# Performance work log

Measured on AMD Instinct MI355X. Metric: run time of the kernel, lower is better.

The kernel has to match this reference:

```python
import jax, jax.numpy as jnp
import numpy as np

N_KNN = 20
BN_EPS = 1e-5
LRELU_SLOPE = 0.2


def setup_inputs() -> dict:
    key = jax.random.key(0)
    k1, k2, k3 = jax.random.split(key, 3)
    B, C, N = 4, 3, 8192
    x = jax.random.normal(k1, (B, C, N), dtype=jnp.float32)
    # Conv2d(1, 16, 1): weight [16,1,1,1] -> flatten to [16]; bias [16]
    conv_w = jax.random.normal(k2, (16,), dtype=jnp.float32) * (1.0 / np.sqrt(1.0))
    conv_b = jax.random.normal(k3, (16,), dtype=jnp.float32) * 0.01
    gamma = jnp.ones((16,), dtype=jnp.float32)
    beta = jnp.zeros((16,), dtype=jnp.float32)
    return {"x": x, "conv_w": conv_w, "conv_b": conv_b, "gamma": gamma, "beta": beta}


def reference(x, conv_w, conv_b, gamma, beta):
    # x: [B, C, N]
    pts = jnp.transpose(x, (0, 2, 1))  # [B, N, C]
    sq = jnp.sum(pts * pts, axis=-1)  # [B, N]
    # pairwise squared distances, clamped for numerical safety
    d2 = sq[:, :, None] + sq[:, None, :] - 2.0 * jnp.einsum("bnc,bmc->bnm", pts, pts)
    d2 = jnp.maximum(d2, 0.0)
    # safe sqrt: zero gradient at zero distance (matches torch.cdist behavior)
    dist = jnp.where(d2 > 0, jnp.sqrt(jnp.where(d2 > 0, d2, 1.0)), 0.0)  # [B, N, N]
    # k smallest distances = k largest of negated
    neg_topk, _ = jax.lax.top_k(-dist, N_KNN)
    knn = -neg_topk  # [B, N, K], ascending
    # 1x1 conv (1 -> 16 channels): feat[b,c,n,k] = w[c]*knn[b,n,k] + b[c]
    feat = knn[:, None, :, :] * conv_w[None, :, None, None] + conv_b[None, :, None, None]  # [B,16,N,K]
    # BatchNorm2d in training mode: per-channel stats over (B, N, K), biased variance
    mean = jnp.mean(feat, axis=(0, 2, 3), keepdims=True)
    var = jnp.mean((feat - mean) ** 2, axis=(0, 2, 3), keepdims=True)
    xhat = (feat - mean) * jax.lax.rsqrt(var + BN_EPS)
    y = gamma[None, :, None, None] * xhat + beta[None, :, None, None]
    # LeakyReLU(0.2)
    y = jnp.where(y >= 0, y, LRELU_SLOPE * y)
    # max over k neighbors
    return jnp.max(y, axis=-1)  # [B, 16, N]
```

## Files before the change

kernel.cpp:

```cpp
#include <hip/hip_runtime.h>
#include <stdint.h>

#define NPTS  8192
#define NB    4
#define KNN   20
#define NROWS (NB * NPTS)
#define MTOTF 655360.0f
#define WPB   8
#define BLK   (WPB * 64)
#define SLICE (NPTS / WPB)
#define HALF  (NPTS / 2)
#define SLICE2 (HALF / WPB)
#define LSTR  (KNN + 1)
#define CAP   12
#define CAP2  16
#define NEG_INF -3.0e38f

__device__ __forceinline__ float med3f(float a, float b, float c) {
    return __builtin_amdgcn_fmed3f(a, b, c);
}

__device__ __forceinline__ unsigned enc_f(float f) {
    unsigned u = __float_as_uint(f);
    return (u & 0x80000000u) ? ~u : (u | 0x80000000u);
}
__device__ __forceinline__ float dec_f(unsigned u) {
    return __uint_as_float((u & 0x80000000u) ? (u & 0x7fffffffu) : ~u);
}

__device__ __forceinline__ void insert_t(float arr[KNN], float t) {
#pragma unroll
    for (int j = KNN - 1; j > 0; --j) arr[j] = med3f(t, arr[j - 1], arr[j]);
    arr[0] = fmaxf(arr[0], t);
}

__device__ __forceinline__ void flush_buf(float arr[KNN], int& cnt,
    const float* bufw, int lane, unsigned* threshS) {
#pragma unroll
    for (int s = 0; s < CAP; ++s) {
        const float v = bufw[s * 64 + lane];
        insert_t(arr, (s < cnt) ? v : NEG_INF);
    }
    cnt = 0;
    atomicMax(&threshS[lane], enc_f(arr[KNN - 1]));
}

__device__ __forceinline__ void flush_dyn(float arr[KNN], int& cnt,
    const float* bufw, int lane, unsigned* threshS) {
#pragma unroll
    for (int s0 = 0; s0 < CAP2; s0 += 4) {
        if (__any(cnt > s0)) {
#pragma unroll
            for (int s = s0; s < s0 + 4; ++s) {
                const float v = bufw[s * 64 + lane];
                insert_t(arr, (s < cnt) ? v : NEG_INF);
            }
        }
    }
    cnt = 0;
    atomicMax(&threshS[lane], enc_f(arr[KNN - 1]));
}

__device__ __forceinline__ void finalize_row(
    float arr[KNN], float px, float py, float pz, int row, int lane,
    float* __restrict__ kmaxA, float* __restrict__ kminA, float* __restrict__ acc)
{
    const float pn2 = px * px + py * py + pz * pz;
    float sum = 0.f, sum2 = 0.f, dmin = 0.f, dmax = 0.f;
#pragma unroll
    for (int k = 0; k < KNN; ++k) {
        float d2 = fmaxf(fmaf(-2.f, arr[k], pn2), 0.f);
        float d = sqrtf(d2);
        sum += d; sum2 += d2;
        if (k == 0) dmin = d;
        dmax = d;
    }
    kmaxA[row] = dmax;
    kminA[row] = dmin;
#pragma unroll
    for (int o = 32; o; o >>= 1) {
        sum  += __shfl_down(sum,  o, 64);
        sum2 += __shfl_down(sum2, o, 64);
    }
    if (lane == 0) { atomicAdd(acc, sum); atomicAdd(acc + 1, sum2); }
}

__global__ __launch_bounds__(256) void prep_kernel(
    const float* __restrict__ x, float4* __restrict__ tile4, float* __restrict__ acc)
{
    const int i = blockIdx.x * 256 + threadIdx.x;
    const int b = i >> 13;
    const int m = i & (NPTS - 1);
    const float* xb = x + b * 3 * NPTS;
    const float qx = xb[m], qy = xb[NPTS + m], qz = xb[2 * NPTS + m];
    tile4[i] = make_float4(qx, qy, qz, -0.5f * (qx * qx + qy * qy + qz * qz));
    if (i < 2) acc[i] = 0.f;
}

__global__ __launch_bounds__(BLK, 8) void knn_split_kernel(
    const float* __restrict__ x, const float4* __restrict__ tile4,
    float* __restrict__ part)
{
    __shared__ float shmem[(WPB - 1) * 64 * LSTR];
    __shared__ unsigned threshS[64];

    const int tid  = threadIdx.x;
    const int lane = tid & 63;
    const int wave = __builtin_amdgcn_readfirstlane(tid >> 6);
    const int rb   = blockIdx.x >> 1;
    const int half = blockIdx.x & 1;
    const int rowBase = rb * 64;
    const int row  = rowBase + lane;
    const int b    = rowBase >> 13;
    const int n    = row & (NPTS - 1);
    const float* xb = x + b * 3 * NPTS;

    const float px = xb[n];
    const float py = xb[NPTS + n];
    const float pz = xb[2 * NPTS + n];

    if (tid < 64) threshS[tid] = enc_f(NEG_INF);

    float arr[KNN];
#pragma unroll
    for (int j = 0; j < KNN; ++j) arr[j] = NEG_INF;

    float* bufw = shmem + wave * (CAP2 * 64);
    __syncthreads();

    const float4* __restrict__ tp = tile4 + b * NPTS + half * HALF + wave * SLICE2;

#pragma unroll 8
    for (int i = 0; i < 32; ++i) {
        const float4 q = tp[i];
        insert_t(arr, fmaf(q.x, px, fmaf(q.y, py, fmaf(q.z, pz, q.w))));
    }
    atomicMax(&threshS[lane], enc_f(arr[KNN - 1]));

    int cnt = 0;
    for (int c = 1; c < SLICE2 / 32; ++c) {
        float th = dec_f(*(volatile unsigned*)(threshS + lane));
        const float4* tq = tp + c * 32;
        for (int g = 0; g < 8; ++g) {
#pragma unroll
            for (int u = 0; u < 4; ++u) {
                const float4 q = tq[g * 4 + u];
                const float t = fmaf(q.x, px, fmaf(q.y, py, fmaf(q.z, pz, q.w)));
                bufw[cnt * 64 + lane] = t;
                cnt += (t > th);
            }
            if (__any(cnt > CAP2 - 4)) {
                flush_dyn(arr, cnt, bufw, lane, threshS);
                th = dec_f(*(volatile unsigned*)(threshS + lane));
            }
        }
    }
    if (__any(cnt > 0)) flush_dyn(arr, cnt, bufw, lane, threshS);
    __syncthreads();

    if (wave > 0) {
        float* dst = shmem + ((wave - 1) * 64 + lane) * LSTR;
#pragma unroll
        for (int j = 0; j < KNN; ++j) dst[j] = arr[j];
    }
    __syncthreads();

    if (wave == 0) {
        for (int wsrc = 0; wsrc < WPB - 1; ++wsrc) {
            const float* src = shmem + (wsrc * 64 + lane) * LSTR;
#pragma unroll
            for (int k = 0; k < KNN; ++k) insert_t(arr, src[k]);
        }
        float4* dst = (float4*)(part + (row * 2 + half) * KNN);
#pragma unroll
        for (int k = 0; k < KNN; k += 4)
            dst[k >> 2] = make_float4(arr[k], arr[k + 1], arr[k + 2], arr[k + 3]);
    }
}

__global__ __launch_bounds__(256) void merge_kernel(
    const float* __restrict__ x, const float* __restrict__ part,
    float* __restrict__ kmaxA, float* __restrict__ kminA, float* __restrict__ acc)
{
    const int r = blockIdx.x * 256 + threadIdx.x;
    const int lane = threadIdx.x & 63;
    const int b = r >> 13;
    const int n = r & (NPTS - 1);
    const float* xb = x + b * 3 * NPTS;
    const float px = xb[n];
    const float py = xb[NPTS + n];
    const float pz = xb[2 * NPTS + n];

    const float4* pA = (const float4*)(part + r * 2 * KNN);
    float arr[KNN];
#pragma unroll
    for (int k = 0; k < KNN; k += 4) {
        const float4 v = pA[k >> 2];
        arr[k] = v.x; arr[k + 1] = v.y; arr[k + 2] = v.z; arr[k + 3] = v.w;
    }
#pragma unroll
    for (int k = 0; k < KNN; k += 4) {
        const float4 v = pA[(KNN + k) >> 2];
        insert_t(arr, v.x); insert_t(arr, v.y); insert_t(arr, v.z); insert_t(arr, v.w);
    }
    finalize_row(arr, px, py, pz, r, lane, kmaxA, kminA, acc);
}

__global__ __launch_bounds__(BLK, 8) void knn_kernel(
    const float* __restrict__ x, const float4* __restrict__ tile4,
    float* __restrict__ kmaxA, float* __restrict__ kminA, float* __restrict__ acc)
{
    __shared__ float shmem[(WPB - 1) * 64 * LSTR];
    __shared__ unsigned threshS[64];

    const int tid  = threadIdx.x;
    const int lane = tid & 63;
    const int wave = __builtin_amdgcn_readfirstlane(tid >> 6);
    const int rowBase = blockIdx.x * 64;
    const int row  = rowBase + lane;
    const int b    = rowBase >> 13;
    const int n    = row & (NPTS - 1);
    const float* xb = x + b * 3 * NPTS;

    const float px = xb[n];
    const float py = xb[NPTS + n];
    const float pz = xb[2 * NPTS + n];

    if (tid < 64) threshS[tid] = enc_f(NEG_INF);

    float arr[KNN];
#pragma unroll
    for (int j = 0; j < KNN; ++j) arr[j] = NEG_INF;

    float* bufw = shmem + wave * (CAP * 64);
    int cnt = 0;
    __syncthreads();

    const float4* __restrict__ tp = tile4 + b * NPTS + wave * SLICE;
    float th = NEG_INF;
    for (int c = 0; c < SLICE / 32; ++c) {
        th = dec_f(*(volatile unsigned*)(threshS + lane));
        const float4* tq = tp + c * 32;
        for (int g = 0; g < 8; ++g) {
#pragma unroll
            for (int u = 0; u < 4; ++u) {
                const float4 q = tq[g * 4 + u];
                const float t = fmaf(q.x, px, fmaf(q.y, py, fmaf(q.z, pz, q.w)));
                if (t > th) { bufw[cnt * 64 + lane] = t; ++cnt; }
            }
            if (__any(cnt > CAP - 4)) {
                flush_buf(arr, cnt, bufw, lane, threshS);
                th = dec_f(*(volatile unsigned*)(threshS + lane));
            }
        }
    }
    if (__any(cnt > 0)) flush_buf(arr, cnt, bufw, lane, threshS);
    __syncthreads();

    if (wave > 0) {
        float* dst = shmem + ((wave - 1) * 64 + lane) * LSTR;
#pragma unroll
        for (int j = 0; j < KNN; ++j) dst[j] = arr[j];
    }
    __syncthreads();

    if (wave == 0) {
        for (int wsrc = 0; wsrc < WPB - 1; ++wsrc) {
            const float* src = shmem + (wsrc * 64 + lane) * LSTR;
#pragma unroll
            for (int k = 0; k < KNN; ++k) insert_t(arr, src[k]);
        }
        finalize_row(arr, px, py, pz, row, lane, kmaxA, kminA, acc);
    }
}

__global__ __launch_bounds__(BLK) void knn_kernel_lds(
    const float* __restrict__ x,
    float* __restrict__ kmaxA, float* __restrict__ kminA, float* __restrict__ acc)
{
    __shared__ float4 tile[2048];
    __shared__ float  lists[(WPB - 1) * 64 * LSTR];

    const int tid  = threadIdx.x;
    const int lane = tid & 63;
    const int wave = tid >> 6;
    const int rowBase = blockIdx.x * 64;
    const int row  = rowBase + lane;
    const int b    = rowBase >> 13;
    const int n    = row & (NPTS - 1);
    const float* xb = x + b * 3 * NPTS;

    const float px = xb[n];
    const float py = xb[NPTS + n];
    const float pz = xb[2 * NPTS + n];

    float arr[KNN];
#pragma unroll
    for (int j = 0; j < KNN; ++j) arr[j] = NEG_INF;

    for (int t0 = 0; t0 < NPTS; t0 += 2048) {
        __syncthreads();
        const int i4 = tid * 4;
        const float4 qx4 = *(const float4*)(xb + t0 + i4);
        const float4 qy4 = *(const float4*)(xb + NPTS + t0 + i4);
        const float4 qz4 = *(const float4*)(xb + 2 * NPTS + t0 + i4);
        tile[i4 + 0] = make_float4(qx4.x, qy4.x, qz4.x, -0.5f * (qx4.x*qx4.x + qy4.x*qy4.x + qz4.x*qz4.x));
        tile[i4 + 1] = make_float4(qx4.y, qy4.y, qz4.y, -0.5f * (qx4.y*qx4.y + qy4.y*qy4.y + qz4.y*qz4.y));
        tile[i4 + 2] = make_float4(qx4.z, qy4.z, qz4.z, -0.5f * (qx4.z*qx4.z + qy4.z*qy4.z + qz4.z*qz4.z));
        tile[i4 + 3] = make_float4(qx4.w, qy4.w, qz4.w, -0.5f * (qx4.w*qx4.w + qy4.w*qy4.w + qz4.w*qz4.w));
        __syncthreads();
        const float4* base = tile + wave * 256;
#pragma unroll 4
        for (int i = 0; i < 256; ++i) {
            const float4 q = base[i];
            float t = fmaf(q.x, px, fmaf(q.y, py, fmaf(q.z, pz, q.w)));
            insert_t(arr, t);
        }
    }
    __syncthreads();

    if (wave > 0) {
        float* dst = lists + ((wave - 1) * 64 + lane) * LSTR;
#pragma unroll
        for (int j = 0; j < KNN; ++j) dst[j] = arr[j];
    }
    __syncthreads();

    if (wave == 0) {
        for (int wsrc = 0; wsrc < WPB - 1; ++wsrc) {
            const float* src = lists + (wsrc * 64 + lane) * LSTR;
#pragma unroll
            for (int k = 0; k < KNN; ++k) insert_t(arr, src[k]);
        }
        finalize_row(arr, px, py, pz, row, lane, kmaxA, kminA, acc);
    }
}

__global__ __launch_bounds__(256) void out_kernel(
    const float* __restrict__ kmaxA, const float* __restrict__ kminA,
    const float* __restrict__ acc,
    const float* __restrict__ w, const float* __restrict__ gamma,
    const float* __restrict__ beta, float* __restrict__ out)
{
    const int r = blockIdx.x * 256 + threadIdx.x;
    const int b = r >> 13;
    const int n = r & (NPTS - 1);
    const float mu  = acc[0] * (1.0f / MTOTF);
    float var = acc[1] * (1.0f / MTOTF) - mu * mu;
    var = fmaxf(var, 0.f);
    const float kmax = kmaxA[r];
    const float kmin = kminA[r];
#pragma unroll
    for (int c = 0; c < 16; ++c) {
        const float wc = w[c];
        const float a = gamma[c] * wc * rsqrtf(wc * wc * var + 1e-5f);
        const float d = beta[c] - a * mu;
        float v = a * (a >= 0.f ? kmax : kmin) + d;
        v = (v >= 0.f) ? v : 0.2f * v;
        out[(b * 16 + c) * NPTS + n] = v;
    }
}

extern "C" void kernel_launch(void* const* d_in, const int* in_sizes, int n_in,
                              void* d_out, int out_size, void* d_ws, size_t ws_size,
                              hipStream_t stream)
{
    const float* x     = (const float*)d_in[0];
    const float* w     = (const float*)d_in[1];
    const float* gamma = (const float*)d_in[3];
    const float* beta  = (const float*)d_in[4];
    float* out = (float*)d_out;
    float* ws  = (float*)d_ws;

    float* kmaxA = ws;
    float* kminA = ws + NROWS;
    float* acc   = ws + 2 * NROWS;
    float4* tile4 = (float4*)(ws + 2 * NROWS + 4);
    float* part = ws + (2 * NROWS + 4) + 4 * NROWS;
    const size_t need_tile  = (size_t)(2 * NROWS + 4) * 4 + (size_t)NROWS * 16;
    const size_t need_split = need_tile + (size_t)NROWS * 2 * KNN * 4;

    if (ws_size >= need_split) {
        prep_kernel<<<NROWS / 256, 256, 0, stream>>>(x, tile4, acc);
        knn_split_kernel<<<2 * (NROWS / 64), BLK, 0, stream>>>(x, tile4, part);
        merge_kernel<<<NROWS / 256, 256, 0, stream>>>(x, part, kmaxA, kminA, acc);
    } else if (ws_size >= need_tile) {
        prep_kernel<<<NROWS / 256, 256, 0, stream>>>(x, tile4, acc);
        knn_kernel<<<NROWS / 64, BLK, 0, stream>>>(x, tile4, kmaxA, kminA, acc);
    } else {
        prep_kernel<<<1, 256, 0, stream>>>(x, tile4, acc);
        knn_kernel_lds<<<NROWS / 64, BLK, 0, stream>>>(x, kmaxA, kminA, acc);
    }
    out_kernel<<<NROWS / 256, 256, 0, stream>>>(kmaxA, kminA, acc, w, gamma, beta, out);
}
```

Measured before the change: 202.5 us.

## Replace per-wave flush buffers with shared hot list drained round-robin

Each row's top-k now lives in one shared ladder in LDS with a shared threshold. Candidates above the threshold go into a fixed per-wave hot buffer, and one wave per phase drains all waves' buffers into the ladder while the others keep scanning. Overflow falls back to per-lane register lists that are merged at the end. The aim is to cut the repeated per-wave insertion sorts and the final 8-way merge, at the cost of 16 block barriers, a serial drain by one wave each phase, and benign races on the hot buffer.

Result: slower. 428.5 us (+111.6%).

```diff
diff --git a/kernel.cpp b/kernel.cpp
--- a/kernel.cpp
+++ b/kernel.cpp
@@ -13,8 +13,11 @@
 #define SLICE2 (HALF / WPB)
 #define LSTR  (KNN + 1)
 #define CAP   12
-#define CAP2  16
+#define CW    14
+#define WARM  32
+#define NPH   15
 #define NEG_INF -3.0e38f
+#define SENTU 0x7fbfffffu
 
 __device__ __forceinline__ float med3f(float a, float b, float c) {
     return __builtin_amdgcn_fmed3f(a, b, c);
@@ -45,20 +48,40 @@
     atomicMax(&threshS[lane], enc_f(arr[KNN - 1]));
 }
 
-__device__ __forceinline__ void flush_dyn(float arr[KNN], int& cnt,
-    const float* bufw, int lane, unsigned* threshS) {
-#pragma unroll
-    for (int s0 = 0; s0 < CAP2; s0 += 4) {
-        if (__any(cnt > s0)) {
-#pragma unroll
-            for (int s = s0; s < s0 + 4; ++s) {
-                const float v = bufw[s * 64 + lane];
-                insert_t(arr, (s < cnt) ? v : NEG_INF);
-            }
-        }
-    }
-    cnt = 0;
-    atomicMax(&threshS[lane], enc_f(arr[KNN - 1]));
+__device__ __forceinline__ void drain_rows(
+    const float* hotS, float* ladS, float* threshS, int* curS, int lane)
+{
+    float lad[KNN];
+#pragma unroll
+    for (int k = 0; k < KNN; ++k) lad[k] = ladS[lane * LSTR + k];
+    for (int w = 0; w < WPB; ++w) {
+        int cur = curS[w * 64 + lane];
+        while (true) {
+            bool act = cur < CW;
+            float v = NEG_INF;
+            if (act) v = hotS[(w * CW + cur) * 64 + lane];
+            act = act && (__float_as_uint(v) != SENTU);
+            if (!__any(act)) break;
+            if (act) { insert_t(lad, v); ++cur; }
+        }
+        curS[w * 64 + lane] = cur;
+    }
+#pragma unroll
+    for (int k = 0; k < KNN; ++k) ladS[lane * LSTR + k] = lad[k];
+    threshS[lane] = lad[KNN - 1];
+}
+
+__device__ __forceinline__ void merge_arr_to_lad(
+    float* ladS, float* threshS, const float arr[KNN], int lane)
+{
+    float lad[KNN];
+#pragma unroll
+    for (int k = 0; k < KNN; ++k) lad[k] = ladS[lane * LSTR + k];
+#pragma unroll
+    for (int k = 0; k < KNN; ++k) insert_t(lad, arr[k]);
+#pragma unroll
+    for (int k = 0; k < KNN; ++k) ladS[lane * LSTR + k] = lad[k];
+    threshS[lane] = lad[KNN - 1];
 }
 
 __device__ __forceinline__ void finalize_row(
@@ -97,12 +120,15 @@
     if (i < 2) acc[i] = 0.f;
 }
 
-__global__ __launch_bounds__(BLK, 8) void knn_split_kernel(
+__global__ __launch_bounds__(BLK, 8) void knn_hot_kernel(
     const float* __restrict__ x, const float4* __restrict__ tile4,
     float* __restrict__ part)
 {
-    __shared__ float shmem[(WPB - 1) * 64 * LSTR];
-    __shared__ unsigned threshS[64];
+    __shared__ float    hotS[WPB * CW * 64];
+    __shared__ float    ladS[64 * LSTR];
+    __shared__ float    threshS[64];
+    __shared__ int      curS[WPB * 64];
+    __shared__ unsigned dirtyS;
 
     const int tid  = threadIdx.x;
     const int lane = tid & 63;
@@ -114,67 +140,83 @@
     const int b    = rowBase >> 13;
     const int n    = row & (NPTS - 1);
     const float* xb = x + b * 3 * NPTS;
-
     const float px = xb[n];
     const float py = xb[NPTS + n];
     const float pz = xb[2 * NPTS + n];
 
-    if (tid < 64) threshS[tid] = enc_f(NEG_INF);
+    for (int i = tid; i < WPB * CW * 64; i += BLK) ((unsigned*)hotS)[i] = SENTU;
+    for (int i = tid; i < WPB * 64; i += BLK) curS[i] = 0;
+    if (tid == 0) dirtyS = 0u;
 
     float arr[KNN];
 #pragma unroll
     for (int j = 0; j < KNN; ++j) arr[j] = NEG_INF;
 
-    float* bufw = shmem + wave * (CAP2 * 64);
-    __syncthreads();
-
     const float4* __restrict__ tp = tile4 + b * NPTS + half * HALF + wave * SLICE2;
 
-#pragma unroll 8
-    for (int i = 0; i < 32; ++i) {
+#pragma unroll 4
+    for (int i = 0; i < WARM; ++i) {
         const float4 q = tp[i];
         insert_t(arr, fmaf(q.x, px, fmaf(q.y, py, fmaf(q.z, pz, q.w))));
     }
-    atomicMax(&threshS[lane], enc_f(arr[KNN - 1]));
-
+
+    for (int w = 0; w < WPB; ++w) {
+        __syncthreads();
+        if (wave == w) {
+            if (w == 0) {
+#pragma unroll
+                for (int k = 0; k < KNN; ++k) ladS[lane * LSTR + k] = arr[k];
+                threshS[lane] = arr[KNN - 1];
+            } else {
+                merge_arr_to_lad(ladS, threshS, arr, lane);
+            }
+        }
+    }
+    __syncthreads();
+
+#pragma unroll
+    for (int j = 0; j < KNN; ++j) arr[j] = NEG_INF;
+
+    float* secp = &hotS[(wave * CW) * 64 + lane];
     int cnt = 0;
-    for (int c = 1; c < SLICE2 / 32; ++c) {
-        float th = dec_f(*(volatile unsigned*)(threshS + lane));
-        const float4* tq = tp + c * 32;
-        for (int g = 0; g < 8; ++g) {
-#pragma unroll
-            for (int u = 0; u < 4; ++u) {
-                const float4 q = tq[g * 4 + u];
-                const float t = fmaf(q.x, px, fmaf(q.y, py, fmaf(q.z, pz, q.w)));
-                bufw[cnt * 64 + lane] = t;
-                cnt += (t > th);
+
+    for (int p = 0; p < NPH; ++p) {
+        const float th = threshS[lane];
+        if (wave == (p & 7))
+            drain_rows(hotS, ladS, threshS, curS, lane);
+        const float4* tq = tp + WARM + p * 32;
+#pragma unroll 4
+        for (int i = 0; i < 32; ++i) {
+            const float4 q = tq[i];
+            const float t = fmaf(q.x, px, fmaf(q.y, py, fmaf(q.z, pz, q.w)));
+            if (t > th) {
+                if (cnt < CW) { secp[cnt * 64] = t; ++cnt; }
+                else { insert_t(arr, t); atomicOr(&dirtyS, 1u); }
             }
-            if (__any(cnt > CAP2 - 4)) {
-                flush_dyn(arr, cnt, bufw, lane, threshS);
-                th = dec_f(*(volatile unsigned*)(threshS + lane));
-            }
-        }
-    }
-    if (__any(cnt > 0)) flush_dyn(arr, cnt, bufw, lane, threshS);
-    __syncthreads();
-
-    if (wave > 0) {
-        float* dst = shmem + ((wave - 1) * 64 + lane) * LSTR;
-#pragma unroll
-        for (int j = 0; j < KNN; ++j) dst[j] = arr[j];
+        }
+        __syncthreads();
+    }
+
+    if (wave == 7) drain_rows(hotS, ladS, threshS, curS, lane);
+    __syncthreads();
+
+    if (dirtyS) {
+        for (int w = 0; w < WPB; ++w) {
+            __syncthreads();
+            if (wave == w && __any(arr[0] != NEG_INF))
+                merge_arr_to_lad(ladS, threshS, arr, lane);
+        }
     }
     __syncthreads();
 
     if (wave == 0) {
-        for (int wsrc = 0; wsrc < WPB - 1; ++wsrc) {
-            const float* src = shmem + (wsrc * 64 + lane) * LSTR;
-#pragma unroll
-            for (int k = 0; k < KNN; ++k) insert_t(arr, src[k]);
-        }
+        float o[KNN];
+#pragma unroll
+        for (int k = 0; k < KNN; ++k) o[k] = ladS[lane * LSTR + k];
         float4* dst = (float4*)(part + (row * 2 + half) * KNN);
 #pragma unroll
         for (int k = 0; k < KNN; k += 4)
-            dst[k >> 2] = make_float4(arr[k], arr[k + 1], arr[k + 2], arr[k + 3]);
+            dst[k >> 2] = make_float4(o[k], o[k + 1], o[k + 2], o[k + 3]);
     }
 }
 
@@ -382,7 +424,7 @@
 
     if (ws_size >= need_split) {
         prep_kernel<<<NROWS / 256, 256, 0, stream>>>(x, tile4, acc);
-        knn_split_kernel<<<2 * (NROWS / 64), BLK, 0, stream>>>(x, tile4, part);
+        knn_hot_kernel<<<2 * (NROWS / 64), BLK, 0, stream>>>(x, tile4, part);
         merge_kernel<<<NROWS / 256, 256, 0, stream>>>(x, part, kmaxA, kminA, acc);
     } else if (ws_size >= need_tile) {
         prep_kernel<<<NROWS / 256, 256, 0, stream>>>(x, tile4, acc);
```

## Pack candidate points in pairs for packed FMA and tree-merge wave results

Applied to the files above, without the earlier changes.

Prep now writes candidate points as interleaved pairs (x0,x1,y0,y1 / z0,z1,w0,w1) so the KNN kernel can score two candidates with packed two-wide FMAs. Pairs are staged and filtered together against the threshold using the max of the two scores, and flushed with a smaller per-wave buffer. The final cross-wave merge becomes a log-depth tree instead of wave 0 serially merging seven lists. This aims to cut the distance arithmetic and the serial merge tail. The cost is more extra inserts when only one element of a pair passes, plus more block barriers.

New measurement: 212.6 us. +5.0%, slower.

```diff
diff --git a/kernel.cpp b/kernel.cpp
--- a/kernel.cpp
+++ b/kernel.cpp
@@ -13,11 +13,24 @@
 #define SLICE2 (HALF / WPB)
 #define LSTR  (KNN + 1)
 #define CAP   12
-#define CAP2  16
+#define CW2   8
+#define PWARM 16
+#define PPH   16
+#define NPH2  ((SLICE2 / 2 - PWARM) / PPH)
 #define NEG_INF -3.0e38f
+
+typedef float f32x2 __attribute__((ext_vector_type(2)));
 
 __device__ __forceinline__ float med3f(float a, float b, float c) {
     return __builtin_amdgcn_fmed3f(a, b, c);
+}
+
+__device__ __forceinline__ f32x2 fma2(f32x2 a, f32x2 b, f32x2 c) {
+#if __has_builtin(__builtin_elementwise_fma)
+    return __builtin_elementwise_fma(a, b, c);
+#else
+    f32x2 r; r.x = fmaf(a.x, b.x, c.x); r.y = fmaf(a.y, b.y, c.y); return r;
+#endif
 }
 
 __device__ __forceinline__ unsigned enc_f(float f) {
@@ -45,15 +58,17 @@
     atomicMax(&threshS[lane], enc_f(arr[KNN - 1]));
 }
 
-__device__ __forceinline__ void flush_dyn(float arr[KNN], int& cnt,
-    const float* bufw, int lane, unsigned* threshS) {
-#pragma unroll
-    for (int s0 = 0; s0 < CAP2; s0 += 4) {
+__device__ __forceinline__ void flush_pairs(float arr[KNN], int& cnt,
+    const f32x2* secp, int lane, unsigned* threshS) {
+#pragma unroll
+    for (int s0 = 0; s0 < CW2; s0 += 2) {
         if (__any(cnt > s0)) {
 #pragma unroll
-            for (int s = s0; s < s0 + 4; ++s) {
-                const float v = bufw[s * 64 + lane];
-                insert_t(arr, (s < cnt) ? v : NEG_INF);
+            for (int s = s0; s < s0 + 2; ++s) {
+                const f32x2 v = secp[s * 64];
+                const bool a = (s < cnt);
+                insert_t(arr, a ? v.x : NEG_INF);
+                insert_t(arr, a ? v.y : NEG_INF);
             }
         }
     }
@@ -97,12 +112,31 @@
     if (i < 2) acc[i] = 0.f;
 }
 
-__global__ __launch_bounds__(BLK, 8) void knn_split_kernel(
+__global__ __launch_bounds__(256) void prep_pair_kernel(
+    const float* __restrict__ x, float4* __restrict__ tile4, float* __restrict__ acc)
+{
+    const int p = blockIdx.x * 256 + threadIdx.x;
+    const int b = p >> 12;
+    const int j = p & (NPTS / 2 - 1);
+    const float* xb = x + b * 3 * NPTS;
+    const f32x2 xx = *(const f32x2*)(xb + 2 * j);
+    const f32x2 yy = *(const f32x2*)(xb + NPTS + 2 * j);
+    const f32x2 zz = *(const f32x2*)(xb + 2 * NPTS + 2 * j);
+    const float w0 = -0.5f * (xx.x * xx.x + yy.x * yy.x + zz.x * zz.x);
+    const float w1 = -0.5f * (xx.y * xx.y + yy.y * yy.y + zz.y * zz.y);
+    tile4[2 * p + 0] = make_float4(xx.x, xx.y, yy.x, yy.y);
+    tile4[2 * p + 1] = make_float4(zz.x, zz.y, w0, w1);
+    if (p < 2) acc[p] = 0.f;
+}
+
+__global__ __launch_bounds__(BLK, 8) void knn_pk_kernel(
     const float* __restrict__ x, const float4* __restrict__ tile4,
     float* __restrict__ part)
 {
-    __shared__ float shmem[(WPB - 1) * 64 * LSTR];
+    __shared__ __align__(16) char smem[WPB * CW2 * 64 * sizeof(f32x2)];
     __shared__ unsigned threshS[64];
+    f32x2* hot = (f32x2*)smem;
+    float* ml  = (float*)smem;
 
     const int tid  = threadIdx.x;
     const int lane = tid & 63;
@@ -114,63 +148,91 @@
     const int b    = rowBase >> 13;
     const int n    = row & (NPTS - 1);
     const float* xb = x + b * 3 * NPTS;
-
     const float px = xb[n];
     const float py = xb[NPTS + n];
     const float pz = xb[2 * NPTS + n];
+    const f32x2 px2 = {px, px}, py2 = {py, py}, pz2 = {pz, pz};
 
     if (tid < 64) threshS[tid] = enc_f(NEG_INF);
 
     float arr[KNN];
 #pragma unroll
     for (int j = 0; j < KNN; ++j) arr[j] = NEG_INF;
-
-    float* bufw = shmem + wave * (CAP2 * 64);
-    __syncthreads();
-
-    const float4* __restrict__ tp = tile4 + b * NPTS + half * HALF + wave * SLICE2;
-
-#pragma unroll 8
-    for (int i = 0; i < 32; ++i) {
-        const float4 q = tp[i];
-        insert_t(arr, fmaf(q.x, px, fmaf(q.y, py, fmaf(q.z, pz, q.w))));
+    __syncthreads();
+
+    const f32x2* __restrict__ q2 = (const f32x2*)tile4;
+    const int pbase = b * (NPTS / 2) + half * (HALF / 2) + wave * (SLICE2 / 2);
+
+#pragma unroll 4
+    for (int i = 0; i < PWARM; ++i) {
+        const f32x2* tq = q2 + 4 * (pbase + i);
+        const f32x2 r = fma2(tq[0], px2, fma2(tq[1], py2, fma2(tq[2], pz2, tq[3])));
+        insert_t(arr, r.x);
+        insert_t(arr, r.y);
     }
     atomicMax(&threshS[lane], enc_f(arr[KNN - 1]));
 
+    f32x2* secp = hot + (wave * CW2) * 64 + lane;
     int cnt = 0;
-    for (int c = 1; c < SLICE2 / 32; ++c) {
+
+    for (int p = 0; p < NPH2; ++p) {
         float th = dec_f(*(volatile unsigned*)(threshS + lane));
-        const float4* tq = tp + c * 32;
-        for (int g = 0; g < 8; ++g) {
+        const f32x2* tq = q2 + 4 * (pbase + PWARM + p * PPH);
+        for (int g = 0; g < 4; ++g) {
 #pragma unroll
             for (int u = 0; u < 4; ++u) {
-                const float4 q = tq[g * 4 + u];
-                const float t = fmaf(q.x, px, fmaf(q.y, py, fmaf(q.z, pz, q.w)));
-                bufw[cnt * 64 + lane] = t;
-                cnt += (t > th);
+                const int j = g * 4 + u;
+                const f32x2 ax = tq[4 * j + 0];
+                const f32x2 ay = tq[4 * j + 1];
+                const f32x2 az = tq[4 * j + 2];
+                const f32x2 aw = tq[4 * j + 3];
+                const f32x2 r = fma2(ax, px2, fma2(ay, py2, fma2(az, pz2, aw)));
+                secp[cnt * 64] = r;
+                cnt += (fmaxf(r.x, r.y) > th);
             }
-            if (__any(cnt > CAP2 - 4)) {
-                flush_dyn(arr, cnt, bufw, lane, threshS);
+            if (__any(cnt > CW2 - 4)) {
+                flush_pairs(arr, cnt, secp, lane, threshS);
                 th = dec_f(*(volatile unsigned*)(threshS + lane));
             }
         }
     }
-    if (__any(cnt > 0)) flush_dyn(arr, cnt, bufw, lane, threshS);
-    __syncthreads();
-
-    if (wave > 0) {
-        float* dst = shmem + ((wave - 1) * 64 + lane) * LSTR;
-#pragma unroll
-        for (int j = 0; j < KNN; ++j) dst[j] = arr[j];
-    }
-    __syncthreads();
-
+    if (__any(cnt > 0)) flush_pairs(arr, cnt, secp, lane, threshS);
+    __syncthreads();
+
+    if (wave & 1) {
+        float* d = ml + (wave >> 1) * (64 * LSTR) + lane * LSTR;
+#pragma unroll
+        for (int k = 0; k < KNN; ++k) d[k] = arr[k];
+    }
+    __syncthreads();
+    if (!(wave & 1)) {
+        const float* s = ml + (wave >> 1) * (64 * LSTR) + lane * LSTR;
+#pragma unroll
+        for (int k = 0; k < KNN; ++k) insert_t(arr, s[k]);
+    }
+    __syncthreads();
+    if (!(wave & 1) && (wave & 2)) {
+        float* d = ml + (wave >> 2) * (64 * LSTR) + lane * LSTR;
+#pragma unroll
+        for (int k = 0; k < KNN; ++k) d[k] = arr[k];
+    }
+    __syncthreads();
+    if ((wave & 3) == 0) {
+        const float* s = ml + (wave >> 2) * (64 * LSTR) + lane * LSTR;
+#pragma unroll
+        for (int k = 0; k < KNN; ++k) insert_t(arr, s[k]);
+    }
+    __syncthreads();
+    if (wave == 4) {
+        float* d = ml + lane * LSTR;
+#pragma unroll
+        for (int k = 0; k < KNN; ++k) d[k] = arr[k];
+    }
+    __syncthreads();
     if (wave == 0) {
-        for (int wsrc = 0; wsrc < WPB - 1; ++wsrc) {
-            const float* src = shmem + (wsrc * 64 + lane) * LSTR;
-#pragma unroll
-            for (int k = 0; k < KNN; ++k) insert_t(arr, src[k]);
-        }
+        const float* s = ml + lane * LSTR;
+#pragma unroll
+        for (int k = 0; k < KNN; ++k) insert_t(arr, s[k]);
         float4* dst = (float4*)(part + (row * 2 + half) * KNN);
 #pragma unroll
         for (int k = 0; k < KNN; k += 4)
@@ -381,8 +443,8 @@
     const size_t need_split = need_tile + (size_t)NROWS * 2 * KNN * 4;
 
     if (ws_size >= need_split) {
-        prep_kernel<<<NROWS / 256, 256, 0, stream>>>(x, tile4, acc);
-        knn_split_kernel<<<2 * (NROWS / 64), BLK, 0, stream>>>(x, tile4, part);
+        prep_pair_kernel<<<NROWS / 512, 256, 0, stream>>>(x, tile4, acc);
+        knn_pk_kernel<<<2 * (NROWS / 64), BLK, 0, stream>>>(x, tile4, part);
         merge_kernel<<<NROWS / 256, 256, 0, stream>>>(x, part, kmaxA, kminA, acc);
     } else if (ws_size >= need_tile) {
         prep_kernel<<<NROWS / 256, 256, 0, stream>>>(x, tile4, acc);
```

## Fuse prep, split KNN, merge and output into one cooperative kernel

Applied to the files above, without the earlier changes.

Adds a cooperative mega-kernel that runs the prep, split KNN search, merge/finalize and output phases in one launch, separated by grid-wide syncs. It tries the cooperative launch first and falls back to the old multi-kernel path if that launch fails. The goal is to remove the launch overhead and gaps between the four kernels. The cost is that NGRID=1024 blocks of 512 threads must all be resident at once, which limits occupancy and adds grid-sync overhead. If residency is not possible the launch fails and the old path runs.

New measurement: 507.1 us. 150% more time.

```diff
diff --git a/kernel.cpp b/kernel.cpp
--- a/kernel.cpp
+++ b/kernel.cpp
@@ -1,5 +1,8 @@
 #include <hip/hip_runtime.h>
+#include <hip/hip_cooperative_groups.h>
 #include <stdint.h>
+
+namespace cg = cooperative_groups;
 
 #define NPTS  8192
 #define NB    4
@@ -14,6 +17,7 @@
 #define LSTR  (KNN + 1)
 #define CAP   12
 #define CAP2  16
+#define NGRID (2 * (NROWS / 64))
 #define NEG_INF -3.0e38f
 
 __device__ __forceinline__ float med3f(float a, float b, float c) {
@@ -84,6 +88,171 @@
     }
     if (lane == 0) { atomicAdd(acc, sum); atomicAdd(acc + 1, sum2); }
 }
+
+__global__ __launch_bounds__(BLK, 8) void mega_kernel(
+    const float* __restrict__ x, const float* __restrict__ w,
+    const float* __restrict__ gamma, const float* __restrict__ beta,
+    float4* __restrict__ tile4, float* __restrict__ part,
+    float* __restrict__ kmaxA, float* __restrict__ kminA,
+    float* __restrict__ acc, float* __restrict__ out)
+{
+    cg::grid_group grid = cg::this_grid();
+    __shared__ float shmem[WPB * CAP2 * 64];
+    __shared__ unsigned threshS[64];
+
+    const int tid  = threadIdx.x;
+    const int lane = tid & 63;
+    const int wave = __builtin_amdgcn_readfirstlane(tid >> 6);
+    const int blk  = blockIdx.x;
+
+    if (blk < NROWS / BLK) {
+        const int i = blk * BLK + tid;
+        const int b = i >> 13;
+        const int m = i & (NPTS - 1);
+        const float* xb = x + b * 3 * NPTS;
+        const float qx = xb[m], qy = xb[NPTS + m], qz = xb[2 * NPTS + m];
+        tile4[i] = make_float4(qx, qy, qz, -0.5f * (qx * qx + qy * qy + qz * qz));
+        if (i < 2) acc[i] = 0.f;
+    }
+    grid.sync();
+
+    {
+        const int rb   = blk >> 1;
+        const int half = blk & 1;
+        const int rowBase = rb * 64;
+        const int row  = rowBase + lane;
+        const int b    = rowBase >> 13;
+        const int n    = row & (NPTS - 1);
+        const float* xb = x + b * 3 * NPTS;
+        const float px = xb[n];
+        const float py = xb[NPTS + n];
+        const float pz = xb[2 * NPTS + n];
+
+        if (tid < 64) threshS[tid] = enc_f(NEG_INF);
+
+        float arr[KNN];
+#pragma unroll
+        for (int j = 0; j < KNN; ++j) arr[j] = NEG_INF;
+        float* bufw = shmem + wave * (CAP2 * 64);
+        __syncthreads();
+
+        const float4* __restrict__ tp = tile4 + b * NPTS + half * HALF + wave * SLICE2;
+
+#pragma unroll 8
+        for (int i = 0; i < 32; ++i) {
+            const float4 q = tp[i];
+            insert_t(arr, fmaf(q.x, px, fmaf(q.y, py, fmaf(q.z, pz, q.w))));
+        }
+        atomicMax(&threshS[lane], enc_f(arr[KNN - 1]));
+
+        int cnt = 0;
+        for (int c = 1; c < SLICE2 / 32; ++c) {
+            float th = dec_f(*(volatile unsigned*)(threshS + lane));
+            const float4* tq = tp + c * 32;
+            for (int g = 0; g < 8; ++g) {
+#pragma unroll
+                for (int u = 0; u < 4; ++u) {
+                    const float4 q = tq[g * 4 + u];
+                    const float t = fmaf(q.x, px, fmaf(q.y, py, fmaf(q.z, pz, q.w)));
+                    bufw[cnt * 64 + lane] = t;
+                    cnt += (t > th);
+                }
+                if (__any(cnt > CAP2 - 4)) {
+                    flush_dyn(arr, cnt, bufw, lane, threshS);
+                    th = dec_f(*(volatile unsigned*)(threshS + lane));
+                }
+            }
+        }
+        if (__any(cnt > 0)) flush_dyn(arr, cnt, bufw, lane, threshS);
+        __syncthreads();
+
+        float* ml = shmem;
+        if (wave & 1) {
+            float* d = ml + (wave >> 1) * (64 * LSTR) + lane * LSTR;
+#pragma unroll
+            for (int k = 0; k < KNN; ++k) d[k] = arr[k];
+        }
+        __syncthreads();
+        if (!(wave & 1)) {
+            const float* s = ml + (wave >> 1) * (64 * LSTR) + lane * LSTR;
+#pragma unroll
+            for (int k = 0; k < KNN; ++k) insert_t(arr, s[k]);
+        }
+        __syncthreads();
+        if (!(wave & 1) && (wave & 2)) {
+            float* d = ml + (wave >> 2) * (64 * LSTR) + lane * LSTR;
+#pragma unroll
+            for (int k = 0; k < KNN; ++k) d[k] = arr[k];
+        }
+        __syncthreads();
+        if ((wave & 3) == 0) {
+            const float* s = ml + (wave >> 2) * (64 * LSTR) + lane * LSTR;
+#pragma unroll
+            for (int k = 0; k < KNN; ++k) insert_t(arr, s[k]);
+        }
+        __syncthreads();
+        if (wave == 4) {
+            float* d = ml + lane * LSTR;
+#pragma unroll
+            for (int k = 0; k < KNN; ++k) d[k] = arr[k];
+        }
+        __syncthreads();
+        if (wave == 0) {
+            const float* s = ml + lane * LSTR;
+#pragma unroll
+            for (int k = 0; k < KNN; ++k) insert_t(arr, s[k]);
+            float4* dst = (float4*)(part + (row * 2 + half) * KNN);
+#pragma unroll
+            for (int k = 0; k < KNN; k += 4)
+                dst[k >> 2] = make_float4(arr[k], arr[k + 1], arr[k + 2], arr[k + 3]);
+        }
+    }
+    grid.sync();
+
+    if (blk < NROWS / BLK) {
+        const int r = blk * BLK + tid;
+        const int b = r >> 13;
+        const int n = r & (NPTS - 1);
+        const float* xb = x + b * 3 * NPTS;
+        const float px = xb[n];
+        const float py = xb[NPTS + n];
+        const float pz = xb[2 * NPTS + n];
+
+        const float4* pA = (const float4*)(part + r * 2 * KNN);
+        float arr[KNN];
+#pragma unroll
+        for (int k = 0; k < KNN; k += 4) {
+            const float4 v = pA[k >> 2];
+            arr[k] = v.x; arr[k + 1] = v.y; arr[k + 2] = v.z; arr[k + 3] = v.w;
+        }
+#pragma unroll
+        for (int k = 0; k < KNN; k += 4) {
+            const float4 v = pA[(KNN + k) >> 2];
+            insert_t(arr, v.x); insert_t(arr, v.y); insert_t(arr, v.z); insert_t(arr, v.w);
+        }
+        finalize_row(arr, px, py, pz, r, lane, kmaxA, kminA, acc);
+    }
+    grid.sync();
+
+    {
+        const int T = blk * BLK + tid;
+        const int n  = T & (NPTS - 1);
+        const int bc = T >> 13;
+        const int c  = bc & 15;
+        const int b  = bc >> 4;
+        const float mu  = acc[0] * (1.0f / MTOTF);
+        float var = acc[1] * (1.0f / MTOTF) - mu * mu;
+        var = fmaxf(var, 0.f);
+        const float wc = w[c];
+        const float a  = gamma[c] * wc * rsqrtf(wc * wc * var + 1e-5f);
+        const float d  = beta[c] - a * mu;
+        const float km = (a >= 0.f) ? kmaxA[b * NPTS + n] : kminA[b * NPTS + n];
+        float v = a * km + d;
+        v = (v >= 0.f) ? v : 0.2f * v;
+        out[T] = v;
+    }
+}
+
 
 __global__ __launch_bounds__(256) void prep_kernel(
     const float* __restrict__ x, float4* __restrict__ tile4, float* __restrict__ acc)
@@ -114,7 +283,6 @@
     const int b    = rowBase >> 13;
     const int n    = row & (NPTS - 1);
     const float* xb = x + b * 3 * NPTS;
-
     const float px = xb[n];
     const float py = xb[NPTS + n];
     const float pz = xb[2 * NPTS + n];
@@ -124,12 +292,10 @@
     float arr[KNN];
 #pragma unroll
     for (int j = 0; j < KNN; ++j) arr[j] = NEG_INF;
-
     float* bufw = shmem + wave * (CAP2 * 64);
     __syncthreads();
 
     const float4* __restrict__ tp = tile4 + b * NPTS + half * HALF + wave * SLICE2;
-
 #pragma unroll 8
     for (int i = 0; i < 32; ++i) {
         const float4 q = tp[i];
@@ -221,7 +387,6 @@
     const int b    = rowBase >> 13;
     const int n    = row & (NPTS - 1);
     const float* xb = x + b * 3 * NPTS;
-
     const float px = xb[n];
     const float py = xb[NPTS + n];
     const float pz = xb[2 * NPTS + n];
@@ -231,7 +396,6 @@
     float arr[KNN];
 #pragma unroll
     for (int j = 0; j < KNN; ++j) arr[j] = NEG_INF;
-
     float* bufw = shmem + wave * (CAP * 64);
     int cnt = 0;
     __syncthreads();
@@ -289,7 +453,6 @@
     const int b    = rowBase >> 13;
     const int n    = row & (NPTS - 1);
     const float* xb = x + b * 3 * NPTS;
-
     const float px = xb[n];
     const float py = xb[NPTS + n];
     const float pz = xb[2 * NPTS + n];
@@ -309,10 +472,10 @@
         tile[i4 + 2] = make_float4(qx4.z, qy4.z, qz4.z, -0.5f * (qx4.z*qx4.z + qy4.z*qy4.z + qz4.z*qz4.z));
         tile[i4 + 3] = make_float4(qx4.w, qy4.w, qz4.w, -0.5f * (qx4.w*qx4.w + qy4.w*qy4.w + qz4.w*qz4.w));
         __syncthreads();
-        const float4* base = tile + wave * 256;
+        const float4* basep = tile + wave * 256;
 #pragma unroll 4
         for (int i = 0; i < 256; ++i) {
-            const float4 q = base[i];
+            const float4 q = basep[i];
             float t = fmaf(q.x, px, fmaf(q.y, py, fmaf(q.z, pz, q.w)));
             insert_t(arr, t);
         }
@@ -376,13 +539,22 @@
     float* kminA = ws + NROWS;
     float* acc   = ws + 2 * NROWS;
     float4* tile4 = (float4*)(ws + 2 * NROWS + 4);
-    float* part = ws + (2 * NROWS + 4) + 4 * NROWS;
+    float* part  = ws + (2 * NROWS + 4) + 4 * NROWS;
     const size_t need_tile  = (size_t)(2 * NROWS + 4) * 4 + (size_t)NROWS * 16;
     const size_t need_split = need_tile + (size_t)NROWS * 2 * KNN * 4;
 
     if (ws_size >= need_split) {
+        void* args[] = {(void*)&x, (void*)&w, (void*)&gamma, (void*)&beta,
+                        (void*)&tile4, (void*)&part, (void*)&kmaxA, (void*)&kminA,
+                        (void*)&acc, (void*)&out};
+        hipError_t e = hipLaunchCooperativeKernel(
+            reinterpret_cast<void*>(mega_kernel),
+            dim3(NGRID), dim3(BLK), args, 0, stream);
+        if (e == hipSuccess) return;
+        (void)hipGetLastError();
+
         prep_kernel<<<NROWS / 256, 256, 0, stream>>>(x, tile4, acc);
-        knn_split_kernel<<<2 * (NROWS / 64), BLK, 0, stream>>>(x, tile4, part);
+        knn_split_kernel<<<NGRID, BLK, 0, stream>>>(x, tile4, part);
         merge_kernel<<<NROWS / 256, 256, 0, stream>>>(x, part, kmaxA, kminA, acc);
     } else if (ws_size >= need_tile) {
         prep_kernel<<<NROWS / 256, 256, 0, stream>>>(x, tile4, acc);
```
